# Kernel optimization log

Hardware: AMD Instinct MI355X
Metric: run time of the kernel (lower is better)

Reference implementation:

```python
import jax, jax.numpy as jnp
import numpy as np


def setup_inputs() -> dict:
    key = jax.random.key(0)
    k1, k2 = jax.random.split(key)
    B, C, H, W, K = 2, 3, 384, 384, 180
    x = jax.random.normal(k1, (B, C, H, W), dtype=jnp.float32)
    # angles in degrees, uniform over [0, 180)
    angles = jax.random.uniform(k2, (B, K), dtype=jnp.float32) * 180.0
    return {"x": x, "angles": angles}


def _bilinear_sample(img, gy, gx):
    """img: (C,H,W); gy,gx: (K,H,W) normalized coords in [-1,1].
    Emulates torch grid_sample(align_corners=True, mode='bilinear', padding_mode='zeros').
    Returns (C,K,H,W)."""
    H, W = img.shape[1], img.shape[2]
    fx = (gx + 1.0) * 0.5 * (W - 1)
    fy = (gy + 1.0) * 0.5 * (H - 1)
    x0 = jnp.floor(fx)
    y0 = jnp.floor(fy)
    x1 = x0 + 1.0
    y1 = y0 + 1.0
    wx1 = fx - x0
    wx0 = 1.0 - wx1
    wy1 = fy - y0
    wy0 = 1.0 - wy1

    def gather(yi, xi):
        valid = (yi >= 0) & (yi <= H - 1) & (xi >= 0) & (xi <= W - 1)
        yc = jnp.clip(yi, 0, H - 1).astype(jnp.int32)
        xc = jnp.clip(xi, 0, W - 1).astype(jnp.int32)
        v = img[:, yc, xc]  # (C,K,H,W)
        return v * valid[None].astype(img.dtype)

    out = (gather(y0, x0) * (wy0 * wx0)[None]
           + gather(y0, x1) * (wy0 * wx1)[None]
           + gather(y1, x0) * (wy1 * wx0)[None]
           + gather(y1, x1) * (wy1 * wx1)[None])
    return out  # (C,K,H,W)


def reference(x, angles):
    B, C, H, W = x.shape
    K = angles.shape[1]
    xs = jnp.linspace(-1.0, 1.0, W)
    ys = jnp.linspace(-1.0, 1.0, H)
    yy, xx = jnp.meshgrid(ys, xs, indexing='ij')  # (H,W)

    theta = angles * (jnp.pi / 180.0)  # (B,K)
    c = jnp.cos(theta)[..., None, None]  # (B,K,1,1)
    s = jnp.sin(theta)[..., None, None]
    # rot_mat rows: [[c,-s],[s,c]]; out_d = sum_c coords_c * M[c,d]
    gx = xx[None, None] * c + yy[None, None] * s   # (B,K,H,W)
    gy = -xx[None, None] * s + yy[None, None] * c  # (B,K,H,W)

    sampled = jax.vmap(_bilinear_sample)(x, gy, gx)  # (B,C,K,H,W)
    projections = sampled.sum(axis=-1)               # (B,C,K,H) sum over W
    sinogram = jnp.transpose(projections, (0, 1, 3, 2))  # (B,C,H,K)
    return sinogram
```

## Files before the change

kernel.cpp:

```cpp
#include <hip/hip_runtime.h>
#include <hip/hip_fp16.h>
#include <math.h>


constexpr int B = 2, C = 3, H = 384, W = 384, K = 180;
constexpr int TILE = 32;
constexpr int NTW  = W / TILE;
constexpr int NTH  = H / TILE;
constexpr int ROWS = 48;
constexpr int STR  = 68;
constexpr int PLN  = ROWS * STR;

struct Cat { int stage; int xal; int ym; };

__device__ __forceinline__ Cat tile_cat(float A, float Bc, float sth, float cth,
                                        int h0, int tw) {
    const float w0f = (float)(tw * TILE), w1f = w0f + (TILE - 1);
    const float h0f = (float)h0,          h1f = h0f + (TILE - 1);
    const float minfx = A  + fminf(w0f * cth, w1f * cth) + fminf(h0f * sth, h1f * sth);
    const float minfy = Bc + fminf(-w0f * sth, -w1f * sth) + fminf(h0f * cth, h1f * cth);
    Cat c;
    const int xm = (int)floorf(minfx) - 1;
    c.ym  = (int)floorf(minfy) - 1;
    c.xal = xm & ~3;
    const bool skip = (xm + 47 < 0) | (xm > W - 1) | (c.ym + 47 < 0) | (c.ym > H - 1);
    c.stage = skip ? 0 : 1;
    return c;
}

__device__ __forceinline__ void issue_loads(const float* __restrict__ img,
                                            int tid, int xal, int ym,
                                            float4 (&pf)[C][3]) {
    #pragma unroll
    for (int c = 0; c < C; ++c) {
        const float* __restrict__ plane = img + c * (H * W);
        #pragma unroll
        for (int j = 0; j < 3; ++j) {
            const int u = tid + 256 * j;
            const int r = u >> 4;
            const int g = u & 15;
            const int gy = min(max(ym + r, 0), H - 1);
            const int gx = min(max(xal + 4 * g, 0), W - 4);
            pf[c][j] = *reinterpret_cast<const float4*>(plane + gy * W + gx);
        }
    }
}

__device__ __forceinline__ uint32_t pkh2(float a, float b) {
    const __half2 h = __floats2half2_rn(a, b);
    return *reinterpret_cast<const uint32_t*>(&h);
}

__device__ __forceinline__ void write_stage(const float* __restrict__ img,
                                            uint32_t* __restrict__ sm01,
                                            uint32_t* __restrict__ sm2,
                                            int tid, int xal, int ym,
                                            const float4 (&pf)[C][3]) {
    const bool interior = (ym >= 0) & (ym <= H - ROWS) &
                          (xal >= 0) & (xal <= W - 64);
    #pragma unroll
    for (int j = 0; j < 3; ++j) {
        const int u = tid + 256 * j;
        const int r = u >> 4;
        const int g = u & 15;
        const int px = 4 * g;
        const int vc = (r & 7) << 2;
        const int bs = r * STR + (px ^ vc);
        const float4 q0 = pf[0][j];
        const float4 q1 = pf[1][j];
        const float4 q2 = pf[2][j];
        if (interior) {
            const uint4 u01 = make_uint4(pkh2(q0.x, q1.x), pkh2(q0.y, q1.y),
                                         pkh2(q0.z, q1.z), pkh2(q0.w, q1.w));
            const uint4 u2  = make_uint4(pkh2(q2.x, 0.f), pkh2(q2.y, 0.f),
                                         pkh2(q2.z, 0.f), pkh2(q2.w, 0.f));
            *reinterpret_cast<uint4*>(sm01 + bs) = u01;
            *reinterpret_cast<uint4*>(sm2  + bs) = u2;
        } else {
            const int gy = ym + r;
            const bool rowok = ((unsigned)gy < (unsigned)H);
            const int gyc = min(max(gy, 0), H - 1);
            const float* __restrict__ p0 = img + gyc * W;
            const float* __restrict__ p1 = p0 + H * W;
            const float* __restrict__ p2 = p1 + H * W;
            #pragma unroll
            for (int e = 0; e < 4; ++e) {
                const int gxe = xal + px + e;
                const bool ok = rowok && ((unsigned)gxe < (unsigned)W);
                const int gxc = min(max(gxe, 0), W - 1);
                const float t0 = ok ? p0[gxc] : 0.0f;
                const float t1 = ok ? p1[gxc] : 0.0f;
                const float t2 = ok ? p2[gxc] : 0.0f;
                sm01[bs + e] = pkh2(t0, t1);
                sm2 [bs + e] = pkh2(t2, 0.f);
            }
        }
    }
}

__global__ __launch_bounds__(256) void radon_tile(
    const float* __restrict__ x,
    const float* __restrict__ angles,
    float* __restrict__ out)
{
    __shared__ __align__(16) uint32_t smem[2 * PLN];
    uint32_t* sm01 = smem;
    uint32_t* sm2  = smem + PLN;

    const int bid = blockIdx.x;
    const int th  = bid % NTH;
    const int bk  = bid / NTH;
    const int k   = bk % K;
    const int b   = bk / K;

    const int tid = threadIdx.x;
    const int u1  = tid & 31;
    const int u8  = tid >> 5;

    const float theta = angles[b * K + k] * (3.14159265358979323846f / 180.0f);
    float sth, cth;
    sincosf(theta, &sth, &cth);

    const float A  = 0.5f * (W - 1) * (1.0f - cth - sth);
    const float Bc = 0.5f * (H - 1) * (1.0f + sth - cth);

    const bool mapB = fabsf(sth) > fabsf(cth);
    const int wofs = mapB ? u8 : u1;
    const int hofs = mapB ? u1 : u8;
    const float dix = mapB ? 8.0f * cth :  8.0f * sth;
    const float diy = mapB ? -8.0f * sth : 8.0f * cth;

    const int h0 = th * TILE;
    const float hf = (float)(h0 + hofs);

    const float* __restrict__ img = x + (size_t)b * (C * H * W);

    float acc[4][C];
    #pragma unroll
    for (int i = 0; i < 4; ++i)
        #pragma unroll
        for (int c = 0; c < C; ++c) acc[i][c] = 0.0f;

    float4 pf[C][3];
    Cat cur = tile_cat(A, Bc, sth, cth, h0, 0);
    if (cur.stage) issue_loads(img, tid, cur.xal, cur.ym, pf);

    for (int tw = 0; tw < NTW; ++tw) {
        Cat nxt; nxt.stage = 0; nxt.xal = 0; nxt.ym = 0;
        if (tw + 1 < NTW) nxt = tile_cat(A, Bc, sth, cth, h0, tw + 1);

        if (cur.stage) {
            __syncthreads();
            write_stage(img, sm01, sm2, tid, cur.xal, cur.ym, pf);
        }
        if (nxt.stage) issue_loads(img, tid, nxt.xal, nxt.ym, pf);
        if (cur.stage) {
            __syncthreads();
            const float wf = (float)(tw * TILE + wofs);
            float fx = fmaf(hf, sth, fmaf(wf,  cth, A)) - (float)cur.xal;
            float fy = fmaf(hf, cth, fmaf(wf, -sth, Bc)) - (float)cur.ym;
            #pragma unroll
            for (int i = 0; i < 4; ++i) {
                const float xf = floorf(fx), yf = floorf(fy);
                const int lx = (int)xf;
                const int ly = (int)yf;
                const float wx1 = fx - xf, wy1 = fy - yf;
                const float wx0 = 1.0f - wx1, wy0 = 1.0f - wy1;
                const float w00 = wy0 * wx0, w01 = wy0 * wx1;
                const float w10 = wy1 * wx0, w11 = wy1 * wx1;
                const int row0 = ly * STR, row1 = row0 + STR;
                const int v0 = (ly & 7) << 2;
                const int v1 = ((ly + 1) & 7) << 2;
                const int s00 = row0 + ( lx      ^ v0);
                const int s01 = row0 + ((lx + 1) ^ v0);
                const int s10 = row1 + ( lx      ^ v1);
                const int s11 = row1 + ((lx + 1) ^ v1);
                const float2 p00 = __half22float2(*reinterpret_cast<const __half2*>(&sm01[s00]));
                const float2 p01 = __half22float2(*reinterpret_cast<const __half2*>(&sm01[s01]));
                const float2 p10 = __half22float2(*reinterpret_cast<const __half2*>(&sm01[s10]));
                const float2 p11 = __half22float2(*reinterpret_cast<const __half2*>(&sm01[s11]));
                const float2 q00 = __half22float2(*reinterpret_cast<const __half2*>(&sm2[s00]));
                const float2 q01 = __half22float2(*reinterpret_cast<const __half2*>(&sm2[s01]));
                const float2 q10 = __half22float2(*reinterpret_cast<const __half2*>(&sm2[s10]));
                const float2 q11 = __half22float2(*reinterpret_cast<const __half2*>(&sm2[s11]));
                acc[i][0] = fmaf(w00, p00.x, fmaf(w01, p01.x,
                            fmaf(w10, p10.x, fmaf(w11, p11.x, acc[i][0]))));
                acc[i][1] = fmaf(w00, p00.y, fmaf(w01, p01.y,
                            fmaf(w10, p10.y, fmaf(w11, p11.y, acc[i][1]))));
                acc[i][2] = fmaf(w00, q00.x, fmaf(w01, q01.x,
                            fmaf(w10, q10.x, fmaf(w11, q11.x, acc[i][2]))));
                fx += dix; fy += diy;
            }
        }
        cur = nxt;
    }

    if (!mapB) {
        #pragma unroll
        for (int i = 0; i < 4; ++i) {
            #pragma unroll
            for (int c = 0; c < C; ++c) {
                float s = acc[i][c];
                #pragma unroll
                for (int m = 16; m >= 1; m >>= 1) s += __shfl_xor(s, m, 64);
                if (u1 == 0) {
                    const int h = h0 + u8 + 8 * i;
                    out[((size_t)(b * C + c) * H + h) * K + k] = s;
                }
            }
        }
    } else {
        __syncthreads();
        float* red = reinterpret_cast<float*>(smem);
        #pragma unroll
        for (int c = 0; c < C; ++c) {
            const float s = (acc[0][c] + acc[1][c]) + (acc[2][c] + acc[3][c]);
            red[(c * 8 + u8) * 32 + u1] = s;
        }
        __syncthreads();
        if (tid < C * 32) {
            const int c = tid >> 5;
            const int l = tid & 31;
            float s = 0.0f;
            #pragma unroll
            for (int g = 0; g < 8; ++g) s += red[(c * 8 + g) * 32 + l];
            out[((size_t)(b * C + c) * H + (h0 + l)) * K + k] = s;
        }
    }
}

extern "C" void kernel_launch(void* const* d_in, const int* in_sizes, int n_in,
                              void* d_out, int out_size, void* d_ws, size_t ws_size,
                              hipStream_t stream) {
    const float* x      = (const float*)d_in[0];
    const float* angles = (const float*)d_in[1];
    float* out          = (float*)d_out;

    radon_tile<<<B * K * NTH, 256, 0, stream>>>(x, angles, out);
}
```

Before: 251.4 us.

## Double-buffer shared-memory tiles and store channel 2 as fp32

Shared memory now holds two tile buffers, so the stage write for tile t+1 happens while tile t is sampled. This cuts the loop to one barrier per iteration instead of two, and the global loads for tile t+2 are issued ahead of time. Channel 2 is now stored as plain fp32 instead of fp16 packed with a zero, which drops the conversion and improves its precision. Shared memory use doubles to about 52KB per block, which may lower occupancy.

```diff
diff --git a/kernel.cpp b/kernel.cpp
--- a/kernel.cpp
+++ b/kernel.cpp
@@ -10,6 +10,7 @@
 constexpr int ROWS = 48;
 constexpr int STR  = 68;
 constexpr int PLN  = ROWS * STR;
+constexpr int BUFS = 2 * PLN;
 
 struct Cat { int stage; int xal; int ym; };
 
@@ -51,11 +52,12 @@
     return *reinterpret_cast<const uint32_t*>(&h);
 }
 
-__device__ __forceinline__ void write_stage(const float* __restrict__ img,
-                                            uint32_t* __restrict__ sm01,
-                                            uint32_t* __restrict__ sm2,
+__device__ __forceinline__ void write_stage(uint32_t* __restrict__ sb,
+                                            const float* __restrict__ img,
                                             int tid, int xal, int ym,
                                             const float4 (&pf)[C][3]) {
+    uint32_t* __restrict__ sm01 = sb;
+    float*    __restrict__ sm2  = reinterpret_cast<float*>(sb + PLN);
     const bool interior = (ym >= 0) & (ym <= H - ROWS) &
                           (xal >= 0) & (xal <= W - 64);
     #pragma unroll
@@ -72,10 +74,8 @@
         if (interior) {
             const uint4 u01 = make_uint4(pkh2(q0.x, q1.x), pkh2(q0.y, q1.y),
                                          pkh2(q0.z, q1.z), pkh2(q0.w, q1.w));
-            const uint4 u2  = make_uint4(pkh2(q2.x, 0.f), pkh2(q2.y, 0.f),
-                                         pkh2(q2.z, 0.f), pkh2(q2.w, 0.f));
-            *reinterpret_cast<uint4*>(sm01 + bs) = u01;
-            *reinterpret_cast<uint4*>(sm2  + bs) = u2;
+            *reinterpret_cast<uint4*>(sm01 + bs)  = u01;
+            *reinterpret_cast<float4*>(sm2 + bs)  = q2;
         } else {
             const int gy = ym + r;
             const bool rowok = ((unsigned)gy < (unsigned)H);
@@ -92,7 +92,7 @@
                 const float t1 = ok ? p1[gxc] : 0.0f;
                 const float t2 = ok ? p2[gxc] : 0.0f;
                 sm01[bs + e] = pkh2(t0, t1);
-                sm2 [bs + e] = pkh2(t2, 0.f);
+                sm2 [bs + e] = t2;
             }
         }
     }
@@ -103,9 +103,7 @@
     const float* __restrict__ angles,
     float* __restrict__ out)
 {
-    __shared__ __align__(16) uint32_t smem[2 * PLN];
-    uint32_t* sm01 = smem;
-    uint32_t* sm2  = smem + PLN;
+    __shared__ __align__(16) uint32_t smem[2][BUFS];
 
     const int bid = blockIdx.x;
     const int th  = bid % NTH;
@@ -142,23 +140,35 @@
         for (int c = 0; c < C; ++c) acc[i][c] = 0.0f;
 
     float4 pf[C][3];
-    Cat cur = tile_cat(A, Bc, sth, cth, h0, 0);
-    if (cur.stage) issue_loads(img, tid, cur.xal, cur.ym, pf);
-
-    for (int tw = 0; tw < NTW; ++tw) {
-        Cat nxt; nxt.stage = 0; nxt.xal = 0; nxt.ym = 0;
-        if (tw + 1 < NTW) nxt = tile_cat(A, Bc, sth, cth, h0, tw + 1);
-
-        if (cur.stage) {
-            __syncthreads();
-            write_stage(img, sm01, sm2, tid, cur.xal, cur.ym, pf);
-        }
-        if (nxt.stage) issue_loads(img, tid, nxt.xal, nxt.ym, pf);
-        if (cur.stage) {
-            __syncthreads();
-            const float wf = (float)(tw * TILE + wofs);
-            float fx = fmaf(hf, sth, fmaf(wf,  cth, A)) - (float)cur.xal;
-            float fy = fmaf(hf, cth, fmaf(wf, -sth, Bc)) - (float)cur.ym;
+
+    Cat catT = tile_cat(A, Bc, sth, cth, h0, 0);
+    if (catT.stage) {
+        issue_loads(img, tid, catT.xal, catT.ym, pf);
+        write_stage(smem[0], img, tid, catT.xal, catT.ym, pf);
+    }
+    Cat catT1 = tile_cat(A, Bc, sth, cth, h0, 1);
+    if (catT1.stage) issue_loads(img, tid, catT1.xal, catT1.ym, pf);
+
+    for (int t = 0; t < NTW; ++t) {
+        __syncthreads();
+        const int p = t & 1;
+
+        if (t + 1 < NTW && catT1.stage)
+            write_stage(smem[1 - p], img, tid, catT1.xal, catT1.ym, pf);
+
+        Cat catT2; catT2.stage = 0; catT2.xal = 0; catT2.ym = 0;
+        if (t + 2 < NTW) {
+            catT2 = tile_cat(A, Bc, sth, cth, h0, t + 2);
+            if (catT2.stage) issue_loads(img, tid, catT2.xal, catT2.ym, pf);
+        }
+
+        if (catT.stage) {
+            const uint32_t* __restrict__ sm01 = smem[p];
+            const float*    __restrict__ sm2  =
+                reinterpret_cast<const float*>(smem[p] + PLN);
+            const float wf = (float)(t * TILE + wofs);
+            float fx = fmaf(hf, sth, fmaf(wf,  cth, A)) - (float)catT.xal;
+            float fy = fmaf(hf, cth, fmaf(wf, -sth, Bc)) - (float)catT.ym;
             #pragma unroll
             for (int i = 0; i < 4; ++i) {
                 const float xf = floorf(fx), yf = floorf(fy);
@@ -179,20 +189,18 @@
                 const float2 p01 = __half22float2(*reinterpret_cast<const __half2*>(&sm01[s01]));
                 const float2 p10 = __half22float2(*reinterpret_cast<const __half2*>(&sm01[s10]));
                 const float2 p11 = __half22float2(*reinterpret_cast<const __half2*>(&sm01[s11]));
-                const float2 q00 = __half22float2(*reinterpret_cast<const __half2*>(&sm2[s00]));
-                const float2 q01 = __half22float2(*reinterpret_cast<const __half2*>(&sm2[s01]));
-                const float2 q10 = __half22float2(*reinterpret_cast<const __half2*>(&sm2[s10]));
-                const float2 q11 = __half22float2(*reinterpret_cast<const __half2*>(&sm2[s11]));
+                const float c00 = sm2[s00], c01 = sm2[s01];
+                const float c10 = sm2[s10], c11 = sm2[s11];
                 acc[i][0] = fmaf(w00, p00.x, fmaf(w01, p01.x,
                             fmaf(w10, p10.x, fmaf(w11, p11.x, acc[i][0]))));
                 acc[i][1] = fmaf(w00, p00.y, fmaf(w01, p01.y,
                             fmaf(w10, p10.y, fmaf(w11, p11.y, acc[i][1]))));
-                acc[i][2] = fmaf(w00, q00.x, fmaf(w01, q01.x,
-                            fmaf(w10, q10.x, fmaf(w11, q11.x, acc[i][2]))));
+                acc[i][2] = fmaf(w00, c00, fmaf(w01, c01,
+                            fmaf(w10, c10, fmaf(w11, c11, acc[i][2]))));
                 fx += dix; fy += diy;
             }
         }
-        cur = nxt;
+        catT = catT1; catT1 = catT2;
     }
 
     if (!mapB) {
@@ -211,7 +219,7 @@
         }
     } else {
         __syncthreads();
-        float* red = reinterpret_cast<float*>(smem);
+        float* red = reinterpret_cast<float*>(smem[0]);
         #pragma unroll
         for (int c = 0; c < C; ++c) {
             const float s = (acc[0][c] + acc[1][c]) + (acc[2][c] + acc[3][c]);
```

New measurement: 269.6 us. 1.07x slower.
